# Performance work log

Hardware: AMD Instinct MI355X
Metric: run time of the kernel (lower is better)

## Reference

```python
import jax, jax.numpy as jnp
import numpy as np

N = 20000          # num_nodes
R = 48             # num_relations
NB = 12            # num_bases
E = 640000         # num_edges (avg degree 32)
INIT, M1, M2 = 128, 128, 128
OUT3 = 512 - M2 - M1 - INIT  # = 128, per output_size arithmetic in __init__


def setup_inputs() -> dict:
    key = jax.random.key(0)
    ks = jax.random.split(key, 20)
    p = lambda k, shape, s=0.05: jax.random.normal(k, shape, jnp.float32) * s
    return {
        "emb": p(ks[0], (N, INIT)),
        "edge_src": jax.random.randint(ks[1], (E,), 0, N),
        "edge_dst": jax.random.randint(ks[2], (E,), 0, N),
        "edge_types": jax.random.randint(ks[3], (E,), 0, R),
        "comp1": p(ks[4], (R, NB), 0.3), "basis1": p(ks[5], (NB, INIT, M1)),
        "root1": p(ks[6], (INIT, M1)), "bias1": jnp.zeros((M1,), jnp.float32),
        "comp2": p(ks[7], (R, NB), 0.3), "basis2": p(ks[8], (NB, M1, M2)),
        "root2": p(ks[9], (M1, M2)), "bias2": jnp.zeros((M2,), jnp.float32),
        "comp3": p(ks[10], (R, NB), 0.3), "basis3": p(ks[11], (NB, M2, OUT3)),
        "root3": p(ks[12], (M2, OUT3)), "bias3": jnp.zeros((OUT3,), jnp.float32),
    }


def rgcn_conv(x, src, dst, etype, comp, basis, root, bias):
    """PyG RGCNConv with basis decomposition and per-relation mean aggregation.
    out_i = bias + x_i @ root + sum_r W_r^T . mean_{j in N_r(i)} x_j
    Mean aggregation commutes with the linear map, so aggregate raw features per
    (relation, target) first, then apply the relation weights as one batched GEMM.
    """
    Fin = x.shape[1]
    W = jnp.einsum('rb,bio->rio', comp, basis)                 # [R, Fin, Fout]
    seg = etype * N + dst                                      # fused (rel, dst) id
    msg = jax.ops.segment_sum(x[src], seg, num_segments=R * N) # [R*N, Fin]
    cnt = jax.ops.segment_sum(jnp.ones((src.shape[0], 1), x.dtype), seg,
                              num_segments=R * N)
    agg = (msg / jnp.maximum(cnt, 1.0)).reshape(R, N, Fin)     # mean, 0 if no edges
    return jnp.einsum('rni,rio->no', agg, W) + x @ root + bias


def reference(emb, edge_src, edge_dst, edge_types,
              comp1, basis1, root1, bias1,
              comp2, basis2, root2, bias2,
              comp3, basis3, root3, bias3):
    x1 = jax.nn.relu(rgcn_conv(emb, edge_src, edge_dst, edge_types,
                               comp1, basis1, root1, bias1))
    x2 = jax.nn.relu(rgcn_conv(x1, edge_src, edge_dst, edge_types,
                               comp2, basis2, root2, bias2))
    x3 = jax.nn.relu(rgcn_conv(x2, edge_src, edge_dst, edge_types,
                               comp3, basis3, root3, bias3))
    # dropout(0.2) is identity in eval mode
    return jnp.concatenate((x3, x2, x1, emb), axis=1)          # [N, 512]
```

## Files before the change

kernel.cpp:

```cpp
#include <hip/hip_runtime.h>
#include <hip/hip_bf16.h>

#define N_NODES 20000
#define R_REL   48
#define NBASES  12
#define E_EDGES 640000
#define KDIM    1664
#define KSTEPS  52
#define SLOTS   96
#define CPAD    8
#define PF      8

typedef __attribute__((ext_vector_type(8))) short bf16x8;
typedef __attribute__((ext_vector_type(4))) float f32x4;

__device__ inline float loadF(const void* p, long long idx, int isf32) {
    if (isf32 != 0) return ((const float*)p)[idx];
    return __bfloat162float(((const __hip_bfloat16*)p)[idx]);
}

__device__ inline void storeF(void* p, long long idx, int isf32, float v) {
    if (isf32 != 0) ((float*)p)[idx] = v;
    else ((__hip_bfloat16*)p)[idx] = __float2bfloat16(v);
}

__device__ inline unsigned short toBf(float v) {
    __hip_bfloat16 h = __float2bfloat16(v);
    return *(unsigned short*)&h;
}

__global__ void zero_detect(int* p, int n, const void* emb, int* flag) {
    int i = blockIdx.x * 256 + threadIdx.x;
    if (i < n) p[i] = 0;
    if (blockIdx.x == 0 && threadIdx.x == 0) {
        const unsigned short* h = (const unsigned short*)emb;
        int f32 = 0;
        for (int k = 0; k < 256; k++) {
            unsigned int bits = ((unsigned int)h[k]) << 16;
            float v = __uint_as_float(bits);
            if (!(fabsf(v) < 1000.0f)) f32 = 1;
        }
        *flag = f32;
    }
}

__global__ void scatter_d96(const int* src, const int* dst, const int* typ,
                            int* cursordP, int* s_pack) {
    int e = blockIdx.x * 256 + threadIdx.x;
    if (e < E_EDGES) {
        int d = dst[e];
        int pos = atomicAdd(&cursordP[d * CPAD], 1);
        if (pos < SLOTS)
            s_pack[d * SLOTS + pos] = src[e] | (typ[e] << 20);
    }
}

__global__ __launch_bounds__(256) void mkinv(const int* s_pack, const int* cntP,
                                             float* inv48) {
    __shared__ int shcnt[4][R_REL];
    int tid = threadIdx.x;
    int lane = tid & 63;
    int w = tid >> 6;
    int d = blockIdx.x * 4 + w;
    int cnt = cntP[d * CPAD]; if (cnt > SLOTS) cnt = SLOTS;
    int e0 = d * SLOTS;
    int e1 = e0 + cnt;
    if (lane < R_REL) shcnt[w][lane] = 0;
    asm volatile("s_waitcnt lgkmcnt(0)" ::: "memory");
    for (int c0 = e0; c0 < e1; c0 += 64) {
        int e = c0 + lane;
        if (e < e1) atomicAdd(&shcnt[w][s_pack[e] >> 20], 1);
    }
    asm volatile("s_waitcnt lgkmcnt(0) vmcnt(0)" ::: "memory");
    if (lane < R_REL) {
        int c = shcnt[w][lane];
        inv48[(long long)d * R_REL + lane] = (c > 0) ? (1.0f / (float)c) : 0.0f;
    }
}

__global__ void copy_build(const void* b0, const void* r0,
                           const void* b1, const void* r1,
                           const void* b2, const void* r2,
                           __hip_bfloat16* Wt,
                           const void* emb, void* out, float* xc,
                           const int* flagp) {
    int z = blockIdx.z;
    int isf32 = *flagp;
    if (z < 3) {
        const void* basis = (z == 0) ? b0 : (z == 1) ? b1 : b2;
        const void* root  = (z == 0) ? r0 : (z == 1) ? r1 : r2;
        int o = blockIdx.x;
        int k = blockIdx.y * 256 + threadIdx.x;
        if (k >= KDIM) return;
        float v;
        if (k < NBASES * 128) {
            int b = k >> 7, i = k & 127;
            v = loadF(basis, b * 16384 + i * 128 + o, isf32);
        } else {
            v = loadF(root, (k - NBASES * 128) * 128 + o, isf32);
        }
        Wt[(long long)z * (128 * KDIM) + (long long)o * KDIM + k] =
            __float2bfloat16(v);
    } else {
        int base = (blockIdx.y * 128 + blockIdx.x) * 256 + threadIdx.x;
        for (int idx = base; idx < N_NODES * 16; idx += 229376) {
            int n = idx >> 4;
            int c8 = (idx & 15) * 8;
            float4 f0, f1;
            if (isf32) {
                const float4* s = (const float4*)((const float*)emb +
                                                  (long long)n * 128 + c8);
                f0 = s[0]; f1 = s[1];
                float4* d = (float4*)((float*)out +
                                      (long long)n * 512 + 384 + c8);
                d[0] = f0;
                d[1] = f1;
            } else {
                uint4 v = *(const uint4*)((const unsigned short*)emb +
                                          (long long)n * 128 + c8);
                *(uint4*)((unsigned short*)out +
                          (long long)n * 512 + 384 + c8) = v;
                f0.x = __uint_as_float(v.x << 16);
                f0.y = __uint_as_float(v.x & 0xFFFF0000u);
                f0.z = __uint_as_float(v.y << 16);
                f0.w = __uint_as_float(v.y & 0xFFFF0000u);
                f1.x = __uint_as_float(v.z << 16);
                f1.y = __uint_as_float(v.z & 0xFFFF0000u);
                f1.z = __uint_as_float(v.w << 16);
                f1.w = __uint_as_float(v.w & 0xFFFF0000u);
            }
            float4* xd = (float4*)(xc + (long long)n * 128 + c8);
            xd[0] = f0;
            xd[1] = f1;
        }
    }
}

#define FX(j, idx) do {                                                       \
    int p_ = spkw[idx];                                                       \
    pp[j] = p_;                                                               \
    sx[j] = *(const float2*)(xc + (long long)(p_ & 0xFFFFF) * 128 + col);     \
} while (0)

#define CX(j) do {                                                            \
    int rel_ = pp[j] >> 20;                                                   \
    const float* cp_ = &scSw[rel_ * NBASES];                                  \
    float4 cA_ = *(const float4*)cp_;                                         \
    float4 cB_ = *(const float4*)(cp_ + 4);                                   \
    float4 cC_ = *(const float4*)(cp_ + 8);                                   \
    float x0_ = sx[j].x, x1_ = sx[j].y;                                       \
    accA[0]  += cA_.x * x0_;  accB[0]  += cA_.x * x1_;                        \
    accA[1]  += cA_.y * x0_;  accB[1]  += cA_.y * x1_;                        \
    accA[2]  += cA_.z * x0_;  accB[2]  += cA_.z * x1_;                        \
    accA[3]  += cA_.w * x0_;  accB[3]  += cA_.w * x1_;                        \
    accA[4]  += cB_.x * x0_;  accB[4]  += cB_.x * x1_;                        \
    accA[5]  += cB_.y * x0_;  accB[5]  += cB_.y * x1_;                        \
    accA[6]  += cB_.z * x0_;  accB[6]  += cB_.z * x1_;                        \
    accA[7]  += cB_.w * x0_;  accB[7]  += cB_.w * x1_;                        \
    accA[8]  += cC_.x * x0_;  accB[8]  += cC_.x * x1_;                        \
    accA[9]  += cC_.y * x0_;  accB[9]  += cC_.y * x1_;                        \
    accA[10] += cC_.z * x0_;  accB[10] += cC_.z * x1_;                        \
    accA[11] += cC_.w * x0_;  accB[11] += cC_.w * x1_;                        \
} while (0)

__global__ __launch_bounds__(256) void aggregate(
        const int* s_pack, const int* cntP, const float* inv48,
        const void* comp, const float* xc, unsigned short* A,
        const int* flagp) {
    __shared__ float scomp[R_REL * NBASES];
    __shared__ float scS[4][R_REL * NBASES];
    __shared__ int   spk[4][64];
    int isf32 = *flagp;
    int tid = threadIdx.x;
    int lane = tid & 63;
    int w = tid >> 6;
    int dstn = blockIdx.x * 4 + w;

    for (int i = tid; i < R_REL * NBASES; i += 256)
        scomp[i] = loadF(comp, i, isf32);
    __syncthreads();

    int cnt = cntP[dstn * CPAD]; if (cnt > SLOTS) cnt = SLOTS;
    int e0 = dstn * SLOTS;
    int e1 = e0 + cnt;
    int col = lane * 2;
    int* spkw = spk[w];
    float* scSw = scS[w];

    if (lane < R_REL) {
        float iv = inv48[dstn * R_REL + lane];
#pragma unroll
        for (int b = 0; b < NBASES; b++)
            scSw[lane * NBASES + b] = scomp[lane * NBASES + b] * iv;
    }
    asm volatile("s_waitcnt lgkmcnt(0) vmcnt(0)" ::: "memory");

    float accA[NBASES], accB[NBASES];
#pragma unroll
    for (int b = 0; b < NBASES; b++) { accA[b] = 0.0f; accB[b] = 0.0f; }

    for (int c0 = e0; c0 < e1; c0 += 64) {
        {
            int e = c0 + lane;
            spkw[lane] = s_pack[(e < e1) ? e : (e1 - 1)];
        }
        asm volatile("s_waitcnt lgkmcnt(0)" ::: "memory");
        int cn = e1 - c0; if (cn > 64) cn = 64;
        float2 sx[PF]; int pp[PF];
#pragma unroll
        for (int j = 0; j < PF; j++)
            if (j < cn) FX(j, j);
        int i2 = 0;
        for (; i2 + PF <= cn; i2 += PF) {
#pragma unroll
            for (int j = 0; j < PF; j++) {
                CX(j);
                if (i2 + j + PF < cn) FX(j, i2 + j + PF);
            }
        }
#pragma unroll
        for (int j = 0; j < PF; j++)
            if (i2 + j < cn) CX(j);
    }

    unsigned short* Ar = A + (long long)dstn * KDIM;
#pragma unroll
    for (int b = 0; b < NBASES; b++) {
        unsigned int pk = ((unsigned int)toBf(accB[b]) << 16) |
                          (unsigned int)toBf(accA[b]);
        *(unsigned int*)(Ar + b * 128 + col) = pk;
    }
    {
        float2 f = *(const float2*)(xc + (long long)dstn * 128 + col);
        unsigned int pk = ((unsigned int)toBf(f.y) << 16) |
                          (unsigned int)toBf(f.x);
        *(unsigned int*)(Ar + NBASES * 128 + col) = pk;
    }
}

__global__ __launch_bounds__(256) void gemm_out(
        const __hip_bfloat16* A, const __hip_bfloat16* Wt,
        const void* bias, void* out, int slot,
        float* xc, int writeXc, const int* flagp) {
    int isf32 = *flagp;
    int tid = threadIdx.x;
    int lane = tid & 63;
    int w = tid >> 6;
    int lr = lane & 15;
    int lk = lane >> 4;
    int colBase = w * 32;
    int nb = blockIdx.x;
    const __hip_bfloat16* a0p = A + (long long)(nb * 32 + lr) * KDIM;
    const __hip_bfloat16* a1p = a0p + 16 * KDIM;
    const __hip_bfloat16* w0p = Wt + (long long)(colBase + lr) * KDIM;
    const __hip_bfloat16* w1p = w0p + 16 * KDIM;
    f32x4 acc00 = {0.f, 0.f, 0.f, 0.f};
    f32x4 acc01 = {0.f, 0.f, 0.f, 0.f};
    f32x4 acc10 = {0.f, 0.f, 0.f, 0.f};
    f32x4 acc11 = {0.f, 0.f, 0.f, 0.f};
#pragma unroll 4
    for (int ks = 0; ks < KSTEPS; ks++) {
        int ko = ks * 32 + lk * 8;
        bf16x8 a0 = *(const bf16x8*)(a0p + ko);
        bf16x8 a1 = *(const bf16x8*)(a1p + ko);
        bf16x8 b0 = *(const bf16x8*)(w0p + ko);
        bf16x8 b1 = *(const bf16x8*)(w1p + ko);
        acc00 = __builtin_amdgcn_mfma_f32_16x16x32_bf16(a0, b0, acc00, 0, 0, 0);
        acc01 = __builtin_amdgcn_mfma_f32_16x16x32_bf16(a0, b1, acc01, 0, 0, 0);
        acc10 = __builtin_amdgcn_mfma_f32_16x16x32_bf16(a1, b0, acc10, 0, 0, 0);
        acc11 = __builtin_amdgcn_mfma_f32_16x16x32_bf16(a1, b1, acc11, 0, 0, 0);
    }
    float bi0 = loadF(bias, colBase + lr, isf32);
    float bi1 = loadF(bias, colBase + 16 + lr, isf32);
#pragma unroll
    for (int q = 0; q < 4; q++) {
        int row = lk * 4 + q;
        int r0 = nb * 32 + row;
        int r1 = r0 + 16;
        float v00 = fmaxf(acc00[q] + bi0, 0.0f);
        float v01 = fmaxf(acc01[q] + bi1, 0.0f);
        float v10 = fmaxf(acc10[q] + bi0, 0.0f);
        float v11 = fmaxf(acc11[q] + bi1, 0.0f);
        long long n0 = (long long)r0 * 512 + slot;
        long long n1 = (long long)r1 * 512 + slot;
        storeF(out, n0 + colBase + lr,      isf32, v00);
        storeF(out, n0 + colBase + 16 + lr, isf32, v01);
        storeF(out, n1 + colBase + lr,      isf32, v10);
        storeF(out, n1 + colBase + 16 + lr, isf32, v11);
        if (writeXc) {
            xc[(long long)r0 * 128 + colBase + lr]      = v00;
            xc[(long long)r0 * 128 + colBase + 16 + lr] = v01;
            xc[(long long)r1 * 128 + colBase + lr]      = v10;
            xc[(long long)r1 * 128 + colBase + 16 + lr] = v11;
        }
    }
}

extern "C" void kernel_launch(void* const* d_in, const int* in_sizes, int n_in,
                              void* d_out, int out_size, void* d_ws, size_t ws_size,
                              hipStream_t stream) {
    const void* emb  = d_in[0];
    const int* esrc = (const int*)d_in[1];
    const int* edst = (const int*)d_in[2];
    const int* etyp = (const int*)d_in[3];
    const void* comp[3];
    const void* basis[3];
    const void* root[3];
    const void* bias[3];
    for (int l = 0; l < 3; l++) {
        comp[l]  = d_in[4 + l * 4];
        basis[l] = d_in[5 + l * 4];
        root[l]  = d_in[6 + l * 4];
        bias[l]  = d_in[7 + l * 4];
    }

    char* ws = (char*)d_ws;
    int*   flag     = (int*)(ws + 0);
    int*   s_pack   = (int*)(ws + 256);
    int*   cursordP = (int*)(ws + 7680256);
    float* inv48    = (float*)(ws + 8320256);
    __hip_bfloat16* Wt = (__hip_bfloat16*)(ws + 12160256);
    float* xc       = (float*)(ws + 13438208);
    unsigned short* A = (unsigned short*)(ws + 23678208);

    zero_detect<<<625, 256, 0, stream>>>(cursordP, N_NODES * CPAD, emb, flag);
    scatter_d96<<<2500, 256, 0, stream>>>(esrc, edst, etyp, cursordP, s_pack);
    mkinv<<<5000, 256, 0, stream>>>(s_pack, cursordP, inv48);
    copy_build<<<dim3(128, 7, 4), 256, 0, stream>>>(
        basis[0], root[0], basis[1], root[1], basis[2], root[2], Wt,
        emb, d_out, xc, flag);

    const int slots[3] = {256, 128, 0};
    for (int l = 0; l < 3; l++) {
        const __hip_bfloat16* Wtl = Wt + (long long)l * (128 * KDIM);
        aggregate<<<5000, 256, 0, stream>>>(s_pack, cursordP, inv48, comp[l],
                                            xc, A, flag);
        gemm_out<<<625, 256, 0, stream>>>((const __hip_bfloat16*)A, Wtl,
                                          bias[l], d_out, slots[l],
                                          xc, (l < 2) ? 1 : 0, flag);
    }
    (void)in_sizes; (void)n_in; (void)out_size; (void)ws_size;
}
```

Measured before the change: 597.6 us.

## Process edge pairs per wave with float4 gathers and a cross-half reduction

The aggregate kernel now splits each wave into two halves that each take alternate edges, loading 4 feature columns per lane with float4 gathers instead of 2 columns with float2. It keeps 48 accumulators per lane and combines the halves with a shuffle-xor at the end. Odd edge counts are padded with a dummy relation (index 48) whose coefficients are zero, written by mkinv. This aims for wider memory transactions and fewer loop iterations, at the cost of more registers (possible occupancy loss) and an extra reduction step.

```diff
diff --git a/kernel.cpp b/kernel.cpp
--- a/kernel.cpp
+++ b/kernel.cpp
@@ -9,7 +9,7 @@
 #define KSTEPS  52
 #define SLOTS   96
 #define CPAD    8
-#define PF      8
+#define PFP     4
 
 typedef __attribute__((ext_vector_type(8))) short bf16x8;
 typedef __attribute__((ext_vector_type(4))) float f32x4;
@@ -55,7 +55,7 @@
     }
 }
 
-__global__ __launch_bounds__(256) void mkinv(const int* s_pack, const int* cntP,
+__global__ __launch_bounds__(256) void mkinv(int* s_pack, const int* cntP,
                                              float* inv48) {
     __shared__ int shcnt[4][R_REL];
     int tid = threadIdx.x;
@@ -76,6 +76,8 @@
         int c = shcnt[w][lane];
         inv48[(long long)d * R_REL + lane] = (c > 0) ? (1.0f / (float)c) : 0.0f;
     }
+    if (lane == 0 && cnt < SLOTS)
+        s_pack[e0 + cnt] = (R_REL << 20);
 }
 
 __global__ void copy_build(const void* b0, const void* r0,
@@ -136,31 +138,43 @@
     }
 }
 
-#define FX(j, idx) do {                                                       \
-    int p_ = spkw[idx];                                                       \
-    pp[j] = p_;                                                               \
-    sx[j] = *(const float2*)(xc + (long long)(p_ & 0xFFFFF) * 128 + col);     \
+#define FXP(j, pr) do {                                                       \
+    int p_ = spkw[((pr) << 1) | eh];                                          \
+    rl[j] = p_ >> 20;                                                         \
+    sx[j] = *(const float4*)(xc + (long long)(p_ & 0xFFFFF) * 128 + col4);    \
 } while (0)
 
-#define CX(j) do {                                                            \
-    int rel_ = pp[j] >> 20;                                                   \
-    const float* cp_ = &scSw[rel_ * NBASES];                                  \
+#define CXP(j) do {                                                           \
+    const float* cp_ = &scSw[rl[j] * NBASES];                                 \
     float4 cA_ = *(const float4*)cp_;                                         \
     float4 cB_ = *(const float4*)(cp_ + 4);                                   \
     float4 cC_ = *(const float4*)(cp_ + 8);                                   \
-    float x0_ = sx[j].x, x1_ = sx[j].y;                                       \
-    accA[0]  += cA_.x * x0_;  accB[0]  += cA_.x * x1_;                        \
-    accA[1]  += cA_.y * x0_;  accB[1]  += cA_.y * x1_;                        \
-    accA[2]  += cA_.z * x0_;  accB[2]  += cA_.z * x1_;                        \
-    accA[3]  += cA_.w * x0_;  accB[3]  += cA_.w * x1_;                        \
-    accA[4]  += cB_.x * x0_;  accB[4]  += cB_.x * x1_;                        \
-    accA[5]  += cB_.y * x0_;  accB[5]  += cB_.y * x1_;                        \
-    accA[6]  += cB_.z * x0_;  accB[6]  += cB_.z * x1_;                        \
-    accA[7]  += cB_.w * x0_;  accB[7]  += cB_.w * x1_;                        \
-    accA[8]  += cC_.x * x0_;  accB[8]  += cC_.x * x1_;                        \
-    accA[9]  += cC_.y * x0_;  accB[9]  += cC_.y * x1_;                        \
-    accA[10] += cC_.z * x0_;  accB[10] += cC_.z * x1_;                        \
-    accA[11] += cC_.w * x0_;  accB[11] += cC_.w * x1_;                        \
+    float4 x_ = sx[j];                                                        \
+    float cb_;                                                                \
+    cb_ = cA_.x; acc[0]  += cb_*x_.x; acc[1]  += cb_*x_.y;                    \
+                 acc[2]  += cb_*x_.z; acc[3]  += cb_*x_.w;                    \
+    cb_ = cA_.y; acc[4]  += cb_*x_.x; acc[5]  += cb_*x_.y;                    \
+                 acc[6]  += cb_*x_.z; acc[7]  += cb_*x_.w;                    \
+    cb_ = cA_.z; acc[8]  += cb_*x_.x; acc[9]  += cb_*x_.y;                    \
+                 acc[10] += cb_*x_.z; acc[11] += cb_*x_.w;                    \
+    cb_ = cA_.w; acc[12] += cb_*x_.x; acc[13] += cb_*x_.y;                    \
+                 acc[14] += cb_*x_.z; acc[15] += cb_*x_.w;                    \
+    cb_ = cB_.x; acc[16] += cb_*x_.x; acc[17] += cb_*x_.y;                    \
+                 acc[18] += cb_*x_.z; acc[19] += cb_*x_.w;                    \
+    cb_ = cB_.y; acc[20] += cb_*x_.x; acc[21] += cb_*x_.y;                    \
+                 acc[22] += cb_*x_.z; acc[23] += cb_*x_.w;                    \
+    cb_ = cB_.z; acc[24] += cb_*x_.x; acc[25] += cb_*x_.y;                    \
+                 acc[26] += cb_*x_.z; acc[27] += cb_*x_.w;                    \
+    cb_ = cB_.w; acc[28] += cb_*x_.x; acc[29] += cb_*x_.y;                    \
+                 acc[30] += cb_*x_.z; acc[31] += cb_*x_.w;                    \
+    cb_ = cC_.x; acc[32] += cb_*x_.x; acc[33] += cb_*x_.y;                    \
+                 acc[34] += cb_*x_.z; acc[35] += cb_*x_.w;                    \
+    cb_ = cC_.y; acc[36] += cb_*x_.x; acc[37] += cb_*x_.y;                    \
+                 acc[38] += cb_*x_.z; acc[39] += cb_*x_.w;                    \
+    cb_ = cC_.z; acc[40] += cb_*x_.x; acc[41] += cb_*x_.y;                    \
+                 acc[42] += cb_*x_.z; acc[43] += cb_*x_.w;                    \
+    cb_ = cC_.w; acc[44] += cb_*x_.x; acc[45] += cb_*x_.y;                    \
+                 acc[46] += cb_*x_.z; acc[47] += cb_*x_.w;                    \
 } while (0)
 
 __global__ __launch_bounds__(256) void aggregate(
@@ -168,13 +182,15 @@
         const void* comp, const float* xc, unsigned short* A,
         const int* flagp) {
     __shared__ float scomp[R_REL * NBASES];
-    __shared__ float scS[4][R_REL * NBASES];
+    __shared__ float scS[4][(R_REL + 1) * NBASES];
     __shared__ int   spk[4][64];
     int isf32 = *flagp;
     int tid = threadIdx.x;
     int lane = tid & 63;
     int w = tid >> 6;
     int dstn = blockIdx.x * 4 + w;
+    int eh = lane >> 5;
+    int col4 = (lane & 31) * 4;
 
     for (int i = tid; i < R_REL * NBASES; i += 256)
         scomp[i] = loadF(comp, i, isf32);
@@ -183,58 +199,69 @@
     int cnt = cntP[dstn * CPAD]; if (cnt > SLOTS) cnt = SLOTS;
     int e0 = dstn * SLOTS;
     int e1 = e0 + cnt;
-    int col = lane * 2;
+    int cntE = cnt + (cnt & 1);
+    int eLast = e0 + cntE - 1;
     int* spkw = spk[w];
     float* scSw = scS[w];
 
-    if (lane < R_REL) {
-        float iv = inv48[dstn * R_REL + lane];
+    if (lane <= R_REL) {
+        float iv = (lane < R_REL)
+                       ? inv48[(long long)dstn * R_REL + lane] : 0.0f;
+        int lsrc = (lane < R_REL) ? lane : 0;
 #pragma unroll
         for (int b = 0; b < NBASES; b++)
-            scSw[lane * NBASES + b] = scomp[lane * NBASES + b] * iv;
+            scSw[lane * NBASES + b] = scomp[lsrc * NBASES + b] * iv;
     }
     asm volatile("s_waitcnt lgkmcnt(0) vmcnt(0)" ::: "memory");
 
-    float accA[NBASES], accB[NBASES];
-#pragma unroll
-    for (int b = 0; b < NBASES; b++) { accA[b] = 0.0f; accB[b] = 0.0f; }
+    float acc[48];
+#pragma unroll
+    for (int k = 0; k < 48; k++) acc[k] = 0.0f;
 
     for (int c0 = e0; c0 < e1; c0 += 64) {
         {
             int e = c0 + lane;
-            spkw[lane] = s_pack[(e < e1) ? e : (e1 - 1)];
+            spkw[lane] = s_pack[(e < eLast) ? e : eLast];
         }
         asm volatile("s_waitcnt lgkmcnt(0)" ::: "memory");
         int cn = e1 - c0; if (cn > 64) cn = 64;
-        float2 sx[PF]; int pp[PF];
-#pragma unroll
-        for (int j = 0; j < PF; j++)
-            if (j < cn) FX(j, j);
+        int cnP = (cn + 1) >> 1;
+        float4 sx[PFP]; int rl[PFP];
+#pragma unroll
+        for (int j = 0; j < PFP; j++)
+            if (j < cnP) FXP(j, j);
         int i2 = 0;
-        for (; i2 + PF <= cn; i2 += PF) {
-#pragma unroll
-            for (int j = 0; j < PF; j++) {
-                CX(j);
-                if (i2 + j + PF < cn) FX(j, i2 + j + PF);
+        for (; i2 + PFP <= cnP; i2 += PFP) {
+#pragma unroll
+            for (int j = 0; j < PFP; j++) {
+                CXP(j);
+                if (i2 + j + PFP < cnP) FXP(j, i2 + j + PFP);
             }
         }
 #pragma unroll
-        for (int j = 0; j < PF; j++)
-            if (i2 + j < cn) CX(j);
-    }
-
-    unsigned short* Ar = A + (long long)dstn * KDIM;
-#pragma unroll
-    for (int b = 0; b < NBASES; b++) {
-        unsigned int pk = ((unsigned int)toBf(accB[b]) << 16) |
-                          (unsigned int)toBf(accA[b]);
-        *(unsigned int*)(Ar + b * 128 + col) = pk;
-    }
-    {
-        float2 f = *(const float2*)(xc + (long long)dstn * 128 + col);
-        unsigned int pk = ((unsigned int)toBf(f.y) << 16) |
-                          (unsigned int)toBf(f.x);
-        *(unsigned int*)(Ar + NBASES * 128 + col) = pk;
+        for (int j = 0; j < PFP; j++)
+            if (i2 + j < cnP) CXP(j);
+    }
+
+#pragma unroll
+    for (int k = 0; k < 48; k++) acc[k] += __shfl_xor(acc[k], 32);
+
+    if (lane < 32) {
+        unsigned short* Ar = A + (long long)dstn * KDIM;
+#pragma unroll
+        for (int b = 0; b < NBASES; b++) {
+            uint2 pk;
+            pk.x = ((unsigned int)toBf(acc[b * 4 + 1]) << 16) |
+                   (unsigned int)toBf(acc[b * 4 + 0]);
+            pk.y = ((unsigned int)toBf(acc[b * 4 + 3]) << 16) |
+                   (unsigned int)toBf(acc[b * 4 + 2]);
+            *(uint2*)(Ar + b * 128 + col4) = pk;
+        }
+        float4 f = *(const float4*)(xc + (long long)dstn * 128 + col4);
+        uint2 pk;
+        pk.x = ((unsigned int)toBf(f.y) << 16) | (unsigned int)toBf(f.x);
+        pk.y = ((unsigned int)toBf(f.w) << 16) | (unsigned int)toBf(f.z);
+        *(uint2*)(Ar + NBASES * 128 + col4) = pk;
     }
 }
 
```

Measured after the change: 624.0 us. 1.04x slower.
